# Kernel optimization log

Measured on AMD Instinct MI355X. Metric: run time of the kernel, lower is better.

The kernel has to match this reference:

```python
import jax, jax.numpy as jnp
import numpy as np
from jax import lax


def setup_inputs() -> dict:
    key = jax.random.key(0)
    ks = jax.random.split(key, 12)
    B, T_dec, T_enc, E, H, V = 32, 64, 128, 256, 512, 32000
    s = 0.05
    emb_W = jax.random.normal(ks[0], (V, E), jnp.float32) * s
    emb_W = emb_W.at[0].set(0.0)  # padding_idx=0
    return {
        "dec_X": jax.random.randint(ks[1], (B, T_dec), 0, V, dtype=jnp.int64),
        "enc_output": jax.random.normal(ks[2], (B, T_enc, H), jnp.float32),
        "h0": jax.random.normal(ks[3], (1, B, H), jnp.float32),
        "c0": jax.random.normal(ks[4], (1, B, H), jnp.float32),
        "emb_W": emb_W,
        "W_ih": jax.random.normal(ks[5], (4 * H, E), jnp.float32) * s,
        "W_hh": jax.random.normal(ks[6], (4 * H, H), jnp.float32) * s,
        "b_ih": jax.random.normal(ks[7], (4 * H,), jnp.float32) * s,
        "b_hh": jax.random.normal(ks[8], (4 * H,), jnp.float32) * s,
        "attn_W": jax.random.normal(ks[9], (H, 2 * H), jnp.float32) * s,
        "attn_b": jax.random.normal(ks[10], (H,), jnp.float32) * s,
        "fc_W": jax.random.normal(ks[11], (V, H), jnp.float32) * s,
        "fc_b": jnp.zeros((V,), jnp.float32),
    }


def reference(dec_X, enc_output, h0, c0, emb_W, W_ih, W_hh, b_ih, b_hh,
              attn_W, attn_b, fc_W, fc_b):
    # Embedding lookup for all decoder steps at once; padding_idx=0 -> zero vector.
    emb = emb_W[dec_X] * (dec_X != 0)[..., None].astype(emb_W.dtype)  # [B, T_dec, E]
    h, c = h0[0], c0[0]  # [B, H] (num_layers == 1)
    bias = b_ih + b_hh

    def step(carry, x_t):  # x_t: [B, E]
        h, c = carry
        g = x_t @ W_ih.T + h @ W_hh.T + bias          # [B, 4H]
        i, f, gg, o = jnp.split(g, 4, axis=-1)        # torch gate order i,f,g,o
        c = jax.nn.sigmoid(f) * c + jax.nn.sigmoid(i) * jnp.tanh(gg)
        h = jax.nn.sigmoid(o) * jnp.tanh(c)           # dec_rnn_out
        # dot-product attention over encoder timesteps (softmax over dim 1)
        scores = jnp.einsum('bth,bh->bt', enc_output, h)   # [B, T_enc]
        a = jax.nn.softmax(scores, axis=1)
        c_t = jnp.einsum('bt,bth->bh', a, enc_output)       # [B, H]
        cat = jnp.concatenate([h, c_t], axis=-1)            # [B, 2H]
        out = jnp.tanh(cat @ attn_W.T + attn_b)             # [B, H]
        logits = out @ fc_W.T + fc_b                        # [B, V]
        return (h, c), logits

    (h, c), logits = lax.scan(step, (h, c), jnp.swapaxes(emb, 0, 1))
    output = jnp.swapaxes(logits, 0, 1)  # [B, T_dec, V]
    return output, (h[None], c[None])
```

## Files before the change

kernel.cpp:

```cpp
#include <hip/hip_runtime.h>
#include <cstdint>
#include <cstddef>

typedef unsigned short u16;
typedef short s8v __attribute__((ext_vector_type(8)));
typedef float f4v __attribute__((ext_vector_type(4)));

static __device__ __forceinline__ u16 f2bf(float x) {
  union { float f; uint32_t u; } v; v.f = x;
  uint32_t r = v.u + 0x7fffu + ((v.u >> 16) & 1u);
  return (u16)(r >> 16);
}
static __device__ __forceinline__ float sigm(float x) { return 1.0f / (1.0f + __expf(-x)); }

__global__ void kPrep(const float* __restrict__ fcW, const float* __restrict__ attnW,
                      const float* __restrict__ Wih, const float* __restrict__ bih,
                      const float* __restrict__ bhh, const float* __restrict__ embW,
                      const int* __restrict__ decX,
                      u16* __restrict__ fcWb, u16* __restrict__ attnWb, u16* __restrict__ Wihb,
                      u16* __restrict__ embg, float* __restrict__ biassum,
                      int* __restrict__ syncp) {
  const long NF = 16384000L, NA = 524288L, NW = 524288L, NE = 524288L, NB = 2048L, NS = 1024L;
  const long total = NF + NA + NW + NE + NB + NS;
  for (long i = (long)blockIdx.x * blockDim.x + threadIdx.x; i < total;
       i += (long)gridDim.x * blockDim.x) {
    if (i < NF) {
      fcWb[i] = f2bf(fcW[i]);
    } else if (i < NF + NA) {
      long k = i - NF; attnWb[k] = f2bf(attnW[k]);
    } else if (i < NF + NA + NW) {
      long k = i - NF - NA; Wihb[k] = f2bf(Wih[k]);
    } else if (i < NF + NA + NW + NE) {
      long k = i - NF - NA - NW;
      int row = (int)(k >> 8), e = (int)(k & 255);
      int t = row >> 5, b = row & 31;
      int x = decX[b * 64 + t];
      embg[k] = f2bf(embW[(long)x * 256 + e]);
    } else if (i < NF + NA + NW + NE + NB) {
      long k = i - NF - NA - NW - NE;
      biassum[k] = bih[k] + bhh[k];
    } else {
      long k = i - NF - NA - NW - NE - NB;
      syncp[k] = 0;
    }
  }
}

template <int ACT, int OUTBF>
__global__ __launch_bounds__(256) void kGemm(const u16* __restrict__ A, const u16* __restrict__ Bm,
                                             const float* __restrict__ bias,
                                             float* __restrict__ Cf, u16* __restrict__ Cb,
                                             int N, int K) {
  __shared__ u16 lA[8 * 64 * 8];
  __shared__ u16 lB[8 * 64 * 8];
  const int tid = threadIdx.x;
  const int m0 = blockIdx.x * 128, n0 = blockIdx.y * 128;
  const int lane = tid & 63, wid = tid >> 6;
  const int wm = wid >> 1, wn = wid & 1;
  f4v acc[4][4] = {};
  const int nkt = K >> 5;
  for (int kt = 0; kt < nkt; ++kt) {
    const int k0 = kt << 5;
#pragma unroll
    for (int i = 0; i < 2; ++i) {
      int u = i * 256 + tid;
      int m = u >> 2, q = u & 3;
      uint4 va = *(const uint4*)(A + (size_t)(m0 + m) * K + k0 + q * 8);
      *(uint4*)&lA[(((m >> 4) * 64) + q * 16 + (m & 15)) * 8] = va;
      uint4 vb = *(const uint4*)(Bm + (size_t)(n0 + m) * K + k0 + q * 8);
      *(uint4*)&lB[(((m >> 4) * 64) + q * 16 + (m & 15)) * 8] = vb;
    }
    __syncthreads();
    s8v af[4], bfr[4];
#pragma unroll
    for (int i = 0; i < 4; ++i) af[i] = *(const s8v*)&lA[((wm * 4 + i) * 64 + lane) * 8];
#pragma unroll
    for (int j = 0; j < 4; ++j) bfr[j] = *(const s8v*)&lB[((wn * 4 + j) * 64 + lane) * 8];
#pragma unroll
    for (int i = 0; i < 4; ++i)
#pragma unroll
      for (int j = 0; j < 4; ++j)
        acc[i][j] = __builtin_amdgcn_mfma_f32_16x16x32_bf16(af[i], bfr[j], acc[i][j], 0, 0, 0);
    __syncthreads();
  }
  const int rq = lane >> 4, cl = lane & 15;
#pragma unroll
  for (int j = 0; j < 4; ++j) {
    int col = n0 + wn * 64 + j * 16 + cl;
    float bv = bias[col];
#pragma unroll
    for (int i = 0; i < 4; ++i) {
      int rowb = m0 + wm * 64 + i * 16 + rq * 4;
      f4v v = acc[i][j];
#pragma unroll
      for (int r = 0; r < 4; ++r) {
        float x = v[r] + bv;
        if (ACT) x = tanhf(x);
        size_t off = (size_t)(rowb + r) * N + col;
        if (OUTBF) Cb[off] = f2bf(x); else Cf[off] = x;
      }
    }
  }
}

__global__ __launch_bounds__(256, 1) void kLSTM4(const float* __restrict__ Gpre,
                                                 const float* __restrict__ Whh,
                                                 const float* __restrict__ h0,
                                                 const float* __restrict__ c0,
                                                 float* __restrict__ Hall,
                                                 float* __restrict__ hx,
                                                 float* __restrict__ cx,
                                                 int* __restrict__ syncp) {
  __shared__ float4 hl4[5160];
  __shared__ int srank;
  const int tid = threadIdx.x;

  int xcc;
  asm volatile("s_getreg_b32 %0, hwreg(HW_REG_XCC_ID)" : "=s"(xcc));
  xcc &= 7;
  if (tid == 0) srank = atomicAdd(&syncp[xcc * 64], 1);
  __syncthreads();
  const int rank = srank & 31;
  const int j0 = rank * 16;
  const int b0 = xcc * 4;
  int* cnt = &syncp[(8 + xcc) * 64];

  const int jj = tid >> 4;
  const int ks = tid & 15;
  const int g_o = ks >> 2, bb_o = ks & 3;
  const int b_o = b0 + bb_o;
  const int j_o = j0 + jj;
  const bool cellLane = (g_o == 0);

  const float4* W4 = (const float4*)Whh;
  float4 Wr[4][8];
#pragma unroll
  for (int g = 0; g < 4; ++g) {
    const int row = g * 512 + j0 + jj;
#pragma unroll
    for (int i = 0; i < 8; ++i) Wr[g][i] = W4[(size_t)row * 128 + ks + 16 * i];
  }

  float creg = cellLane ? c0[b_o * 512 + j_o] : 0.f;
  const float4* hsrc = (const float4*)h0;
  float gpv = Gpre[(size_t)b_o * 2048 + (size_t)g_o * 512 + j_o];

  for (int t = 0; t < 64; ++t) {
#pragma unroll
    for (int it = 0; it < 2; ++it) {
      int idx = it * 256 + tid;
      int hb = idx >> 7, k4 = idx & 127;
      hl4[idx] = hsrc[(b0 + hb) * 128 + k4];
    }
    __syncthreads();

    float gnext = 0.f;
    if (t < 63)
      gnext = Gpre[((size_t)(t + 1) * 32 + b_o) * 2048 + (size_t)g_o * 512 + j_o];

    float acc[16];
#pragma unroll
    for (int p = 0; p < 16; ++p) acc[p] = 0.f;
#pragma unroll
    for (int i = 0; i < 8; ++i) {
      float4 h4[4];
#pragma unroll
      for (int bb = 0; bb < 4; ++bb) h4[bb] = hl4[bb * 128 + ks + 16 * i];
#pragma unroll
      for (int g = 0; g < 4; ++g) {
        float4 w = Wr[g][i];
#pragma unroll
        for (int bb = 0; bb < 4; ++bb)
          acc[g * 4 + bb] += w.x * h4[bb].x + w.y * h4[bb].y + w.z * h4[bb].z + w.w * h4[bb].w;
      }
    }

#define FOLD_STAGE(OFF, NN)                                        \
    {                                                              \
      const bool hi = (ks & OFF) != 0;                             \
      _Pragma("unroll")                                            \
      for (int q = 0; q < NN; ++q) {                               \
        float keepv = hi ? acc[q + NN] : acc[q];                   \
        float sendv = hi ? acc[q] : acc[q + NN];                   \
        acc[q] = keepv + __shfl_xor(sendv, OFF, 64);               \
      }                                                            \
    }
    FOLD_STAGE(8, 8)
    FOLD_STAGE(4, 4)
    FOLD_STAGE(2, 2)
    FOLD_STAGE(1, 1)
#undef FOLD_STAGE

    float pre = acc[0] + gpv;
    float v = (g_o == 2) ? tanhf(pre) : sigm(pre);
    float fv = __shfl_xor(v, 4, 64);
    float gv = __shfl_xor(v, 8, 64);
    float ov = __shfl_xor(v, 12, 64);
    float* hdst = Hall + (size_t)t * 16384;
    if (cellLane) {
      creg = fv * creg + v * gv;
      float hv = ov * tanhf(creg);
      hdst[b_o * 512 + j_o] = hv;
      if (t == 63) { hx[b_o * 512 + j_o] = hv; cx[b_o * 512 + j_o] = creg; }
    }
    __syncthreads();

    if (t < 63) {
      if (tid == 0) {
        unsigned one = 1u;
        asm volatile("global_atomic_add %0, %1, off"
                     :: "v"(cnt), "v"(one) : "memory");
        const int target = 32 * (t + 1);
        unsigned zero = 0u, old;
        for (;;) {
          asm volatile("global_atomic_add %0, %1, %2, off sc0\n\t"
                       "s_waitcnt vmcnt(0)"
                       : "=v"(old) : "v"(cnt), "v"(zero) : "memory");
          if ((int)old >= target) break;
          __builtin_amdgcn_s_sleep(1);
        }
      }
      __syncthreads();
    }
    gpv = gnext;
    hsrc = (const float4*)hdst;
  }
}

__global__ __launch_bounds__(256) void kAttn(const float* __restrict__ Hall, const float* __restrict__ enc,
                                             u16* __restrict__ CAT) {
  const int bx = blockIdx.x;
  const int b = bx >> 3, tg = bx & 7;
  const int tid = threadIdx.x;
  __shared__ float sh[8][516];
  __shared__ float sa[8][132];
  __shared__ float red[8][32];
  for (int tt = 0; tt < 8; ++tt) {
    int t = tg * 8 + tt;
    const float* hr = Hall + ((size_t)t * 32 + b) * 512;
    u16* cr = CAT + ((size_t)(b * 64 + t)) * 1024;
    for (int k = tid; k < 512; k += 256) { float v = hr[k]; sh[tt][k] = v; cr[k] = f2bf(v); }
  }
  __syncthreads();
  {
    const int tl = tid & 7, eb = tid >> 3;
#pragma unroll
    for (int u = 0; u < 4; ++u) {
      int e = eb + u * 32;
      const float* er = enc + ((size_t)b * 128 + e) * 512;
      float a = 0.f;
      for (int k = 0; k < 512; k += 4) {
        float4 ev = *(const float4*)&er[k];
        float4 hv = *(const float4*)&sh[tl][k];
        a += ev.x * hv.x + ev.y * hv.y + ev.z * hv.z + ev.w * hv.w;
      }
      sa[tl][e] = a;
    }
  }
  __syncthreads();
  {
    const int g = tid >> 5, l = tid & 31;
    float mx = -1e30f;
#pragma unroll
    for (int u = 0; u < 4; ++u) mx = fmaxf(mx, sa[g][l + u * 32]);
    red[g][l] = mx;
    __syncthreads();
    if (l == 0) {
      float m2 = -1e30f;
      for (int i = 0; i < 32; ++i) m2 = fmaxf(m2, red[g][i]);
      sa[g][128] = m2;
    }
    __syncthreads();
    float m2 = sa[g][128];
    float s = 0.f;
#pragma unroll
    for (int u = 0; u < 4; ++u) { int e = l + u * 32; float p = __expf(sa[g][e] - m2); sa[g][e] = p; s += p; }
    red[g][l] = s;
    __syncthreads();
    if (l == 0) {
      float s2 = 0.f;
      for (int i = 0; i < 32; ++i) s2 += red[g][i];
      sa[g][129] = 1.0f / s2;
    }
    __syncthreads();
    float inv = sa[g][129];
#pragma unroll
    for (int u = 0; u < 4; ++u) sa[g][l + u * 32] *= inv;
  }
  __syncthreads();
  {
    float a0[8], a1[8];
#pragma unroll
    for (int tt = 0; tt < 8; ++tt) { a0[tt] = 0.f; a1[tt] = 0.f; }
    const float* eb2 = enc + (size_t)b * 128 * 512 + tid * 2;
    for (int e = 0; e < 128; ++e) {
      float2 v = *(const float2*)&eb2[(size_t)e * 512];
#pragma unroll
      for (int tt = 0; tt < 8; ++tt) { float a = sa[tt][e]; a0[tt] += a * v.x; a1[tt] += a * v.y; }
    }
#pragma unroll
    for (int tt = 0; tt < 8; ++tt) {
      int t = tg * 8 + tt;
      u16* cr = CAT + ((size_t)(b * 64 + t)) * 1024 + 512;
      cr[tid * 2] = f2bf(a0[tt]); cr[tid * 2 + 1] = f2bf(a1[tt]);
    }
  }
}

extern "C" void kernel_launch(void* const* d_in, const int* in_sizes, int n_in,
                              void* d_out, int out_size, void* d_ws, size_t ws_size,
                              hipStream_t stream) {
  const int*   decX  = (const int*)d_in[0];
  const float* enc   = (const float*)d_in[1];
  const float* h0    = (const float*)d_in[2];
  const float* c0    = (const float*)d_in[3];
  const float* embW  = (const float*)d_in[4];
  const float* Wih   = (const float*)d_in[5];
  const float* Whh   = (const float*)d_in[6];
  const float* bih   = (const float*)d_in[7];
  const float* bhh   = (const float*)d_in[8];
  const float* attnW = (const float*)d_in[9];
  const float* attnb = (const float*)d_in[10];
  const float* fcW   = (const float*)d_in[11];
  const float* fcb   = (const float*)d_in[12];
  float* out = (float*)d_out;

  char* ws = (char*)d_ws;
  u16*   fcWb    = (u16*)(ws);
  u16*   attnWb  = (u16*)(ws + 32768000);
  u16*   Wihb    = (u16*)(ws + 33816576);
  u16*   embg    = (u16*)(ws + 34865152);
  float* biassum = (float*)(ws + 35913728);
  float* Gpre    = (float*)(ws + 35921920);
  float* Hall    = (float*)(ws + 52699136);
  u16*   CAT     = (u16*)(ws + 56893440);
  u16*   OUTb    = (u16*)(ws + 61087744);
  int*   syncp   = (int*)(ws + 63184896);

  hipLaunchKernelGGL(kPrep, dim3(4096), dim3(256), 0, stream,
                     fcW, attnW, Wih, bih, bhh, embW, decX, fcWb, attnWb, Wihb, embg, biassum,
                     syncp);
  hipLaunchKernelGGL((kGemm<0, 0>), dim3(16, 16), dim3(256), 0, stream,
                     embg, Wihb, biassum, Gpre, (u16*)nullptr, 2048, 256);
  {
    float* hx = out + 65536000L;
    float* cx = out + 65536000L + 16384L;
    const float* gpreA = Gpre; const float* whhA = Whh;
    const float* h0A = h0;     const float* c0A = c0;
    float* hallA = Hall;       int* syncA = syncp;
    void* args[] = {(void*)&gpreA, (void*)&whhA, (void*)&h0A, (void*)&c0A,
                    (void*)&hallA, (void*)&hx, (void*)&cx, (void*)&syncA};
    hipLaunchCooperativeKernel((void*)kLSTM4, dim3(256), dim3(256), args, 0, stream);
  }
  hipLaunchKernelGGL(kAttn, dim3(256), dim3(256), 0, stream, Hall, enc, CAT);
  hipLaunchKernelGGL((kGemm<1, 1>), dim3(16, 4), dim3(256), 0, stream,
                     CAT, attnWb, attnb, (float*)nullptr, OUTb, 512, 1024);
  hipLaunchKernelGGL((kGemm<0, 0>), dim3(16, 250), dim3(256), 0, stream,
                     OUTb, fcWb, fcb, out, (u16*)nullptr, 32000, 512);
}
```

Baseline: 830.8 us.

## Vectorize prep conversion, use direct global-to-LDS loads, swizzle large GEMM blocks

The prep kernel now converts four floats per thread with vector loads and stores, cutting instruction count in the fp32-to-bf16 weight conversion. The GEMM tile loads use global_load_lds to write straight into LDS, skipping the trip through registers. The LDS addressing is rearranged so each wave's 16-byte lane slots land in the same fragment layout as before. The output-projection GEMM also remaps block IDs so consecutive workgroups are spread across XCD-sized groups, aiming for better cache locality on the fc weights. Both rely on alignment and on how the hardware distributes workgroups.

```diff
diff --git a/kernel.cpp b/kernel.cpp
--- a/kernel.cpp
+++ b/kernel.cpp
@@ -11,7 +11,19 @@
   uint32_t r = v.u + 0x7fffu + ((v.u >> 16) & 1u);
   return (u16)(r >> 16);
 }
+static __device__ __forceinline__ uint2 f2bf4(float4 v) {
+  uint2 r;
+  r.x = (uint32_t)f2bf(v.x) | ((uint32_t)f2bf(v.y) << 16);
+  r.y = (uint32_t)f2bf(v.z) | ((uint32_t)f2bf(v.w) << 16);
+  return r;
+}
 static __device__ __forceinline__ float sigm(float x) { return 1.0f / (1.0f + __expf(-x)); }
+
+typedef __attribute__((address_space(3))) uint32_t lds_u32;
+typedef const __attribute__((address_space(1))) uint32_t glb_u32;
+static __device__ __forceinline__ void gload16(const void* g, void* l) {
+  __builtin_amdgcn_global_load_lds((glb_u32*)g, (lds_u32*)l, 16, 0, 0);
+}
 
 __global__ void kPrep(const float* __restrict__ fcW, const float* __restrict__ attnW,
                       const float* __restrict__ Wih, const float* __restrict__ bih,
@@ -20,33 +32,36 @@
                       u16* __restrict__ fcWb, u16* __restrict__ attnWb, u16* __restrict__ Wihb,
                       u16* __restrict__ embg, float* __restrict__ biassum,
                       int* __restrict__ syncp) {
-  const long NF = 16384000L, NA = 524288L, NW = 524288L, NE = 524288L, NB = 2048L, NS = 1024L;
-  const long total = NF + NA + NW + NE + NB + NS;
+  const long NF4 = 4096000L, NA4 = 131072L, NW4 = 131072L, NE4 = 131072L, NB = 2048L, NS = 1024L;
+  const long total = NF4 + NA4 + NW4 + NE4 + NB + NS;
   for (long i = (long)blockIdx.x * blockDim.x + threadIdx.x; i < total;
        i += (long)gridDim.x * blockDim.x) {
-    if (i < NF) {
-      fcWb[i] = f2bf(fcW[i]);
-    } else if (i < NF + NA) {
-      long k = i - NF; attnWb[k] = f2bf(attnW[k]);
-    } else if (i < NF + NA + NW) {
-      long k = i - NF - NA; Wihb[k] = f2bf(Wih[k]);
-    } else if (i < NF + NA + NW + NE) {
-      long k = i - NF - NA - NW;
-      int row = (int)(k >> 8), e = (int)(k & 255);
+    if (i < NF4) {
+      ((uint2*)fcWb)[i] = f2bf4(((const float4*)fcW)[i]);
+    } else if (i < NF4 + NA4) {
+      long k = i - NF4;
+      ((uint2*)attnWb)[k] = f2bf4(((const float4*)attnW)[k]);
+    } else if (i < NF4 + NA4 + NW4) {
+      long k = i - NF4 - NA4;
+      ((uint2*)Wihb)[k] = f2bf4(((const float4*)Wih)[k]);
+    } else if (i < NF4 + NA4 + NW4 + NE4) {
+      long k = i - NF4 - NA4 - NW4;
+      int row = (int)(k >> 6), e4 = (int)(k & 63);
       int t = row >> 5, b = row & 31;
       int x = decX[b * 64 + t];
-      embg[k] = f2bf(embW[(long)x * 256 + e]);
-    } else if (i < NF + NA + NW + NE + NB) {
-      long k = i - NF - NA - NW - NE;
+      float4 v = *(const float4*)&embW[(long)x * 256 + e4 * 4];
+      ((uint2*)embg)[k] = f2bf4(v);
+    } else if (i < NF4 + NA4 + NW4 + NE4 + NB) {
+      long k = i - NF4 - NA4 - NW4 - NE4;
       biassum[k] = bih[k] + bhh[k];
     } else {
-      long k = i - NF - NA - NW - NE - NB;
+      long k = i - NF4 - NA4 - NW4 - NE4 - NB;
       syncp[k] = 0;
     }
   }
 }
 
-template <int ACT, int OUTBF>
+template <int ACT, int OUTBF, int SWZ>
 __global__ __launch_bounds__(256) void kGemm(const u16* __restrict__ A, const u16* __restrict__ Bm,
                                              const float* __restrict__ bias,
                                              float* __restrict__ Cf, u16* __restrict__ Cb,
@@ -54,7 +69,14 @@
   __shared__ u16 lA[8 * 64 * 8];
   __shared__ u16 lB[8 * 64 * 8];
   const int tid = threadIdx.x;
-  const int m0 = blockIdx.x * 128, n0 = blockIdx.y * 128;
+  int bxx = blockIdx.x, byy = blockIdx.y;
+  if (SWZ) {
+    int id = byy * gridDim.x + bxx;
+    int cpx = (gridDim.x * gridDim.y) >> 3;
+    int l = (id & 7) * cpx + (id >> 3);
+    bxx = l % gridDim.x; byy = l / gridDim.x;
+  }
+  const int m0 = bxx * 128, n0 = byy * 128;
   const int lane = tid & 63, wid = tid >> 6;
   const int wm = wid >> 1, wn = wid & 1;
   f4v acc[4][4] = {};
@@ -63,12 +85,11 @@
     const int k0 = kt << 5;
 #pragma unroll
     for (int i = 0; i < 2; ++i) {
-      int u = i * 256 + tid;
-      int m = u >> 2, q = u & 3;
-      uint4 va = *(const uint4*)(A + (size_t)(m0 + m) * K + k0 + q * 8);
-      *(uint4*)&lA[(((m >> 4) * 64) + q * 16 + (m & 15)) * 8] = va;
-      uint4 vb = *(const uint4*)(Bm + (size_t)(n0 + m) * K + k0 + q * 8);
-      *(uint4*)&lB[(((m >> 4) * 64) + q * 16 + (m & 15)) * 8] = vb;
+      const int d = i * 4 + wid;
+      const int m = (d << 4) | (lane & 15);
+      const int q = lane >> 4;
+      gload16(A + (size_t)(m0 + m) * K + k0 + q * 8, &lA[(i * 256 + wid * 64) * 8]);
+      gload16(Bm + (size_t)(n0 + m) * K + k0 + q * 8, &lB[(i * 256 + wid * 64) * 8]);
     }
     __syncthreads();
     s8v af[4], bfr[4];
@@ -340,7 +361,7 @@
   hipLaunchKernelGGL(kPrep, dim3(4096), dim3(256), 0, stream,
                      fcW, attnW, Wih, bih, bhh, embW, decX, fcWb, attnWb, Wihb, embg, biassum,
                      syncp);
-  hipLaunchKernelGGL((kGemm<0, 0>), dim3(16, 16), dim3(256), 0, stream,
+  hipLaunchKernelGGL((kGemm<0, 0, 0>), dim3(16, 16), dim3(256), 0, stream,
                      embg, Wihb, biassum, Gpre, (u16*)nullptr, 2048, 256);
   {
     float* hx = out + 65536000L;
@@ -353,8 +374,8 @@
     hipLaunchCooperativeKernel((void*)kLSTM4, dim3(256), dim3(256), args, 0, stream);
   }
   hipLaunchKernelGGL(kAttn, dim3(256), dim3(256), 0, stream, Hall, enc, CAT);
-  hipLaunchKernelGGL((kGemm<1, 1>), dim3(16, 4), dim3(256), 0, stream,
+  hipLaunchKernelGGL((kGemm<1, 1, 0>), dim3(16, 4), dim3(256), 0, stream,
                      CAT, attnWb, attnb, (float*)nullptr, OUTb, 512, 1024);
-  hipLaunchKernelGGL((kGemm<0, 0>), dim3(16, 250), dim3(256), 0, stream,
+  hipLaunchKernelGGL((kGemm<0, 0, 1>), dim3(16, 250), dim3(256), 0, stream,
                      OUTb, fcWb, fcb, out, (u16*)nullptr, 32000, 512);
 }
```

After: 854.9 us. 2.9% more time.
